# Kernel optimization log

Measured on AMD Instinct MI355X. Metric: run time of the kernel, lower is better.

The kernel has to match this reference:

```python
import jax, jax.numpy as jnp
import numpy as np

B, T, C, H = 2, 4096, 512, 8
HD = C // H  # head_dim = 64


def setup_inputs() -> dict:
    key = jax.random.key(0)
    ks = jax.random.split(key, 5)
    s = 0.02
    return {
        "x": jax.random.normal(ks[0], (B, T, C), dtype=jnp.float32),
        "Wqkv": jax.random.normal(ks[1], (C, 3 * C), dtype=jnp.float32) * s,
        "bqkv": jax.random.normal(ks[2], (3 * C,), dtype=jnp.float32) * s,
        "Wproj": jax.random.normal(ks[3], (C, C), dtype=jnp.float32) * s,
        "bproj": jax.random.normal(ks[4], (C,), dtype=jnp.float32) * s,
    }


def reference(x, Wqkv, bqkv, Wproj, bproj):
    b, t, c = x.shape
    qkv = x @ Wqkv + bqkv                      # [B,T,3C]
    q, k, v = jnp.split(qkv, 3, axis=-1)
    # [B,T,C] -> [B,H,T,HD]
    q = q.reshape(b, t, H, HD).transpose(0, 2, 1, 3)
    k = k.reshape(b, t, H, HD).transpose(0, 2, 1, 3)
    v = v.reshape(b, t, H, HD).transpose(0, 2, 1, 3)
    att = jnp.einsum("bhqd,bhkd->bhqk", q, k) / jnp.sqrt(jnp.float32(HD))
    causal = jnp.tril(jnp.ones((t, t), dtype=bool))
    att = jnp.where(causal, att, -jnp.inf)
    att = jax.nn.softmax(att, axis=-1)
    y = jnp.einsum("bhqk,bhkd->bhqd", att, v)  # [B,H,T,HD]
    y = y.transpose(0, 2, 1, 3).reshape(b, t, c)
    return y @ Wproj + bproj
```

## Files before the change

### kernel.cpp

```cpp
#include <hip/hip_runtime.h>
#include <math.h>

#define NB 2
#define NT 4096
#define NC 512
#define NH 8
#define ND 64
#define N3C (3*NC)

typedef __attribute__((ext_vector_type(8))) __bf16 bf16x8;
typedef __attribute__((ext_vector_type(4))) __bf16 bf16x4;
typedef __attribute__((ext_vector_type(4))) float  f32x4;

__device__ __forceinline__ void load_lds16(const __bf16* g, __bf16* l) {
    __builtin_amdgcn_global_load_lds(
        (const __attribute__((address_space(1))) void*)g,
        (__attribute__((address_space(3))) void*)l, 16, 0, 0);
}

__device__ __forceinline__ float exp2_fast(float x) {
    return __builtin_amdgcn_exp2f(x);
}

__global__ __launch_bounds__(256) void cvt_bf16_kernel(
    const float* __restrict__ x, __bf16* __restrict__ xb, int n)
{
    const int i = (blockIdx.x * 256 + threadIdx.x) << 3;
    if (i < n) {
        float4 a = *(const float4*)(x + i);
        float4 b = *(const float4*)(x + i + 4);
        bf16x8 o;
        o[0] = (__bf16)a.x; o[1] = (__bf16)a.y; o[2] = (__bf16)a.z; o[3] = (__bf16)a.w;
        o[4] = (__bf16)b.x; o[5] = (__bf16)b.y; o[6] = (__bf16)b.z; o[7] = (__bf16)b.w;
        *(bf16x8*)(xb + i) = o;
    }
}

__global__ __launch_bounds__(256) void prep_kernel(
    const float* __restrict__ Wqkv, const float* __restrict__ Wproj,
    __bf16* __restrict__ wqkvt, __bf16* __restrict__ wprojt)
{
    __shared__ float T[64][65];
    int id = blockIdx.x;
    const float* W; __bf16* Wt; int N, n0, k0;
    if (id < 192) { W = Wqkv;  Wt = wqkvt;  N = N3C; n0 = (id % 24) << 6; k0 = (id / 24) << 6; }
    else { id -= 192; W = Wproj; Wt = wprojt; N = NC;  n0 = (id & 7) << 6;  k0 = (id >> 3) << 6; }
    const int K = NC;

    const int tx = threadIdx.x & 15, ty = threadIdx.x >> 4;
#pragma unroll
    for (int i = 0; i < 4; ++i) {
        const int r = ty + (i << 4);
        float4 v = *(const float4*)(W + (size_t)(k0 + r) * N + n0 + (tx << 2));
        T[r][(tx << 2) + 0] = v.x;
        T[r][(tx << 2) + 1] = v.y;
        T[r][(tx << 2) + 2] = v.z;
        T[r][(tx << 2) + 3] = v.w;
    }
    __syncthreads();
#pragma unroll
    for (int i = 0; i < 4; ++i) {
        const int nr = ty + (i << 4);
        bf16x4 o;
        o[0] = (__bf16)T[(tx << 2) + 0][nr];
        o[1] = (__bf16)T[(tx << 2) + 1][nr];
        o[2] = (__bf16)T[(tx << 2) + 2][nr];
        o[3] = (__bf16)T[(tx << 2) + 3][nr];
        *(bf16x4*)(Wt + (size_t)(n0 + nr) * K + k0 + (tx << 2)) = o;
    }
}

template<int BM>
__global__ __launch_bounds__(256) void gemm_glds_kernel(
    const __bf16* __restrict__ A, const __bf16* __restrict__ Bt,
    const float* __restrict__ bias, void* __restrict__ Cout,
    int M, int N, int K, int out_bf16)
{
    constexpr int IT = BM / 32;
    constexpr int AI = BM / 32;
    __shared__ __align__(16) __bf16 As[BM * 64];
    __shared__ __align__(16) __bf16 Bs[128 * 64];

    const int tid  = threadIdx.x;
    const int w    = tid >> 6, lane = tid & 63;
    const int g    = lane >> 4, n = lane & 15;
    const int n7   = n & 7;
    const int wr   = (w >> 1) * (BM / 2);
    const int wc   = (w & 1) << 6;
    const int m0   = blockIdx.y * BM, n0 = blockIdx.x << 7;

    const __bf16* ag[AI]; __bf16* al[AI];
#pragma unroll
    for (int q = 0; q < AI; ++q) {
        const int G = w * (BM * 2) + q * 64 + lane;
        const int r = G >> 3, pg = G & 7, kg = pg ^ (r & 7);
        ag[q] = A + (size_t)(m0 + r) * K + (kg << 3);
        al[q] = As + ((w * (BM * 2) + q * 64) << 3);
    }
    const __bf16* bg[4]; __bf16* bl[4];
#pragma unroll
    for (int q = 0; q < 4; ++q) {
        const int G = w * 256 + q * 64 + lane;
        const int r = G >> 3, pg = G & 7, kg = pg ^ (r & 7);
        bg[q] = Bt + (size_t)(n0 + r) * K + (kg << 3);
        bl[q] = Bs + ((w * 256 + q * 64) << 3);
    }

    f32x4 acc[IT][4];
#pragma unroll
    for (int i = 0; i < IT; ++i)
#pragma unroll
        for (int j = 0; j < 4; ++j) acc[i][j] = (f32x4){0.f, 0.f, 0.f, 0.f};

    const int ksteps = K >> 6;
    for (int ks = 0; ks < ksteps; ++ks) {
        __syncthreads();
        const int ko = ks << 6;
#pragma unroll
        for (int q = 0; q < AI; ++q) load_lds16(ag[q] + ko, al[q]);
#pragma unroll
        for (int q = 0; q < 4;  ++q) load_lds16(bg[q] + ko, bl[q]);
        __syncthreads();

#pragma unroll
        for (int s = 0; s < 2; ++s) {
            bf16x8 af[IT], bf[4];
#pragma unroll
            for (int i = 0; i < IT; ++i) {
                const int row = wr + (i << 4) + n;
                af[i] = *(const bf16x8*)&As[(row << 6) + ((((s << 2) + g) ^ n7) << 3)];
            }
#pragma unroll
            for (int j = 0; j < 4; ++j) {
                const int row = wc + (j << 4) + n;
                bf[j] = *(const bf16x8*)&Bs[(row << 6) + ((((s << 2) + g) ^ n7) << 3)];
            }
#pragma unroll
            for (int i = 0; i < IT; ++i)
#pragma unroll
                for (int j = 0; j < 4; ++j)
                    acc[i][j] = __builtin_amdgcn_mfma_f32_16x16x32_bf16(af[i], bf[j], acc[i][j], 0, 0, 0);
        }
    }

#pragma unroll
    for (int j = 0; j < 4; ++j) {
        const int colg = n0 + wc + (j << 4) + n;
        const float bb = bias[colg];
#pragma unroll
        for (int i = 0; i < IT; ++i) {
#pragma unroll
            for (int reg = 0; reg < 4; ++reg) {
                const int rowg = m0 + wr + (i << 4) + (g << 2) + reg;
                const float v = acc[i][j][reg] + bb;
                if (out_bf16)
                    ((__bf16*)Cout)[(size_t)rowg * N + colg] = (__bf16)v;
                else
                    ((float*)Cout)[(size_t)rowg * N + colg] = v;
            }
        }
    }
}

__global__ __launch_bounds__(256, 4) void attn_kernel(
    const __bf16* __restrict__ qkv, __bf16* __restrict__ out)
{
    __shared__ __align__(16) unsigned char SMEM[34816];
    __bf16 (*QPs)[72] = (__bf16(*)[72])SMEM;
    __bf16* Ks        = (__bf16*)(SMEM + 9216);
    __bf16 (*Vt)[72]  = (__bf16(*)[72])(SMEM + 25600);

    const int tid  = threadIdx.x;
    const int xi   = blockIdx.x;
    const int bh   = blockIdx.y;
    const int b    = bh >> 3, h = bh & 7;
    const int m    = (bh < 8) ? (63 - xi) : xi;
    const int jt1  = m + 1;

    const int qr0  = m << 6;
    const size_t base = (size_t)b * NT * N3C;
    const int col  = h * ND;

    const int w    = tid >> 6;
    const int lane = tid & 63;
    const int g    = lane >> 4;
    const int n    = lane & 15;
    const int qg   = w >> 1;
    const int kh   = w & 1;
    const int qrow0 = qg << 5;
    const int kcol0 = kh << 5;
    const int sw   = (g ^ (n >> 2)) << 3;

    const int kr = tid >> 3;
    const int kc = (tid & 7) << 3;
    const int vd = lane;
    const int vk = w << 3;

    const __bf16* kg_src[2]; __bf16* kl_dst[2];
#pragma unroll
    for (int q = 0; q < 2; ++q) {
        const int G = w * 128 + q * 64 + lane;
        const int r = G >> 3, pg = G & 7, kgr = pg ^ (r & 7);
        kg_src[q] = qkv + base + NC + col + (size_t)r * N3C + (kgr << 3);
        kl_dst[q] = Ks + ((w * 128 + q * 64) << 3);
    }
    const __bf16* vptr = qkv + base + 2 * NC + col + vd;

#pragma unroll
    for (int i = 0; i < 2; ++i) {
        const int r = kr + (i << 5);
        bf16x8 v = *(const bf16x8*)(qkv + base + (size_t)(qr0 + r) * N3C + col + kc);
        bf16x8 q;
#pragma unroll
        for (int j = 0; j < 8; ++j) q[j] = (__bf16)(0.18033688f * (float)v[j]);
        *(bf16x8*)&QPs[r][kc] = q;
    }

#pragma unroll
    for (int q = 0; q < 2; ++q) load_lds16(kg_src[q], kl_dst[q]);
    __bf16 vreg[16];
#pragma unroll
    for (int j = 0; j < 8; ++j) {
        vreg[j]     = vptr[(size_t)(vk + j) * N3C];
        vreg[8 + j] = vptr[(size_t)(vk + 32 + j) * N3C];
    }
    __syncthreads();

    bf16x8 qf[2][2];
#pragma unroll
    for (int qt = 0; qt < 2; ++qt)
#pragma unroll
        for (int hh = 0; hh < 2; ++hh)
            qf[qt][hh] = *(const bf16x8*)&QPs[qrow0 + (qt << 4) + n][(hh << 5) + (g << 3)];

    bf16x8 ones;
#pragma unroll
    for (int j = 0; j < 8; ++j) ones[j] = (__bf16)1.0f;

    f32x4 O[2][4];
#pragma unroll
    for (int qt = 0; qt < 2; ++qt)
#pragma unroll
        for (int dt = 0; dt < 4; ++dt) O[qt][dt] = (f32x4){0.f, 0.f, 0.f, 0.f};
    f32x4 L[2] = {{0.f,0.f,0.f,0.f},{0.f,0.f,0.f,0.f}};

    for (int jt = 0; jt < jt1; ++jt) {
        __syncthreads();
        {
            bf16x8 va, vb;
#pragma unroll
            for (int j = 0; j < 8; ++j) { va[j] = vreg[j]; vb[j] = vreg[8 + j]; }
            *(bf16x8*)&Vt[vd][vk]      = va;
            *(bf16x8*)&Vt[vd][vk + 32] = vb;
        }
        __syncthreads();

        if (jt + 1 < jt1) {
            const size_t roff = (size_t)((jt + 1) << 6) * N3C;
            const int bo = ((jt + 1) & 1) << 12;
#pragma unroll
            for (int q = 0; q < 2; ++q) load_lds16(kg_src[q] + roff, kl_dst[q] + bo);
            const int kr1 = (jt + 1) << 6;
#pragma unroll
            for (int j = 0; j < 8; ++j) {
                vreg[j]     = vptr[(size_t)(kr1 + vk + j) * N3C];
                vreg[8 + j] = vptr[(size_t)(kr1 + vk + 32 + j) * N3C];
            }
        }

        const __bf16* kb = Ks + ((jt & 1) << 12);
        f32x4 S[2][2];
        __builtin_amdgcn_s_setprio(1);
#pragma unroll
        for (int t = 0; t < 2; ++t) {
            const int row = kcol0 + (t << 4) + n;
            const int r7  = row & 7;
            const bf16x8 k0 = *(const bf16x8*)&kb[(row << 6) + ((g ^ r7) << 3)];
            const bf16x8 k1 = *(const bf16x8*)&kb[(row << 6) + (((g ^ 4) ^ r7) << 3)];
#pragma unroll
            for (int qt = 0; qt < 2; ++qt) {
                f32x4 a = {0.f, 0.f, 0.f, 0.f};
                a = __builtin_amdgcn_mfma_f32_16x16x32_bf16(qf[qt][0], k0, a, 0, 0, 0);
                a = __builtin_amdgcn_mfma_f32_16x16x32_bf16(qf[qt][1], k1, a, 0, 0, 0);
                S[qt][t] = a;
            }
        }
        __builtin_amdgcn_s_setprio(0);

        if (jt == m) {
#pragma unroll
            for (int qt = 0; qt < 2; ++qt)
#pragma unroll
                for (int t = 0; t < 2; ++t)
#pragma unroll
                    for (int reg = 0; reg < 4; ++reg) {
                        const int kg  = (jt << 6) + kcol0 + (t << 4) + n;
                        const int qgl = qr0 + qrow0 + (qt << 4) + (g << 2) + reg;
                        if (kg > qgl) S[qt][t][reg] = -INFINITY;
                    }
        }

#pragma unroll
        for (int qt = 0; qt < 2; ++qt)
#pragma unroll
            for (int t = 0; t < 2; ++t)
#pragma unroll
                for (int reg = 0; reg < 4; ++reg)
                    QPs[qrow0 + (qt << 4) + (g << 2) + reg]
                       [kcol0 + (((t << 4) + n) ^ (g << 3))] =
                        (__bf16)exp2_fast(S[qt][t][reg]);

        bf16x8 vf[4];
#pragma unroll
        for (int dt = 0; dt < 4; ++dt) {
            const int vr = (dt << 4) + n;
            vf[dt] = *(const bf16x8*)&Vt[vr][kcol0 + (g << 3)];
        }

        __builtin_amdgcn_s_setprio(1);
#pragma unroll
        for (int qt = 0; qt < 2; ++qt) {
            const bf16x8 p = *(const bf16x8*)&QPs[qrow0 + (qt << 4) + n][kcol0 + sw];
            L[qt] = __builtin_amdgcn_mfma_f32_16x16x32_bf16(p, ones, L[qt], 0, 0, 0);
#pragma unroll
            for (int dt = 0; dt < 4; ++dt)
                O[qt][dt] = __builtin_amdgcn_mfma_f32_16x16x32_bf16(p, vf[dt], O[qt][dt], 0, 0, 0);
        }
        __builtin_amdgcn_s_setprio(0);
    }

    __syncthreads();
    float* red = (float*)SMEM;
    if (kh == 1) {
#pragma unroll
        for (int qt = 0; qt < 2; ++qt)
#pragma unroll
            for (int reg = 0; reg < 4; ++reg) {
                const int qlx = qrow0 + (qt << 4) + (g << 2) + reg;
#pragma unroll
                for (int dt = 0; dt < 4; ++dt)
                    red[qlx * 64 + (dt << 4) + n] = O[qt][dt][reg];
                if (n == 0) red[4096 + qlx] = L[qt][reg];
            }
    }
    __syncthreads();
    if (kh == 0) {
#pragma unroll
        for (int qt = 0; qt < 2; ++qt)
#pragma unroll
            for (int reg = 0; reg < 4; ++reg) {
                const int qlx = qrow0 + (qt << 4) + (g << 2) + reg;
                const float inv = 1.0f / (L[qt][reg] + red[4096 + qlx]);
                const size_t row = (size_t)b * NT + qr0 + qlx;
#pragma unroll
                for (int dt = 0; dt < 4; ++dt)
                    out[row * NC + col + (dt << 4) + n] =
                        (__bf16)((O[qt][dt][reg] + red[qlx * 64 + (dt << 4) + n]) * inv);
            }
    }
}

extern "C" void kernel_launch(void* const* d_in, const int* in_sizes, int n_in,
                              void* d_out, int out_size, void* d_ws, size_t ws_size,
                              hipStream_t stream)
{
    const float* x     = (const float*)d_in[0];
    const float* Wqkv  = (const float*)d_in[1];
    const float* bqkv  = (const float*)d_in[2];
    const float* Wproj = (const float*)d_in[3];
    const float* bproj = (const float*)d_in[4];
    float* out = (float*)d_out;

    char* ws = (char*)d_ws;
    __bf16* xb     = (__bf16*)(ws);
    __bf16* qkvb   = (__bf16*)(ws + 8388608);
    __bf16* attb   = (__bf16*)(ws + 33554432);
    __bf16* wqkvt  = (__bf16*)(ws + 41943040);
    __bf16* wprojt = (__bf16*)(ws + 43515904);

    cvt_bf16_kernel<<<dim3(2048), dim3(256), 0, stream>>>(x, xb, NB * NT * NC);
    prep_kernel<<<dim3(256), dim3(256), 0, stream>>>(Wqkv, Wproj, wqkvt, wprojt);

    gemm_glds_kernel<128><<<dim3(N3C / 128, (NB * NT) / 128), dim3(256), 0, stream>>>(
        xb, wqkvt, bqkv, qkvb, NB * NT, N3C, NC, 1);

    attn_kernel<<<dim3(64, NB * NH), dim3(256), 0, stream>>>(qkvb, attb);

    gemm_glds_kernel<64><<<dim3(NC / 128, (NB * NT) / 64), dim3(256), 0, stream>>>(
        attb, wprojt, bproj, out, NB * NT, NC, NC, 0);
}
```

Measured before the change: 205.7 us.

## Double-buffer LDS tiles in GEMMs and remap blocks across XCDs

```diff
diff --git a/kernel.cpp b/kernel.cpp
--- a/kernel.cpp
+++ b/kernel.cpp
@@ -71,23 +71,30 @@
 }
 
 template<int BM>
-__global__ __launch_bounds__(256) void gemm_glds_kernel(
+__global__ __launch_bounds__(256) void gemm_db_kernel(
     const __bf16* __restrict__ A, const __bf16* __restrict__ Bt,
     const float* __restrict__ bias, void* __restrict__ Cout,
     int M, int N, int K, int out_bf16)
 {
-    constexpr int IT = BM / 32;
-    constexpr int AI = BM / 32;
-    __shared__ __align__(16) __bf16 As[BM * 64];
-    __shared__ __align__(16) __bf16 Bs[128 * 64];
+    constexpr int IT  = BM / 32;
+    constexpr int AI  = BM / 32;
+    constexpr int ASZ = BM * 64;
+    constexpr int BSZ = 128 * 64;
+    __shared__ __align__(16) __bf16 As[2][ASZ];
+    __shared__ __align__(16) __bf16 Bs[2][BSZ];
 
     const int tid  = threadIdx.x;
     const int w    = tid >> 6, lane = tid & 63;
     const int g    = lane >> 4, n = lane & 15;
-    const int n7   = n & 7;
+    const int n7   = n & 15 & 7;
     const int wr   = (w >> 1) * (BM / 2);
     const int wc   = (w & 1) << 6;
-    const int m0   = blockIdx.y * BM, n0 = blockIdx.x << 7;
+
+    const int nwgx = gridDim.x;
+    const int nwg  = nwgx * gridDim.y;
+    const int flat = blockIdx.y * nwgx + blockIdx.x;
+    const int s    = (flat & 7) * (nwg >> 3) + (flat >> 3);
+    const int m0   = (s / nwgx) * BM, n0 = (s % nwgx) << 7;
 
     const __bf16* ag[AI]; __bf16* al[AI];
 #pragma unroll
@@ -95,7 +102,7 @@
         const int G = w * (BM * 2) + q * 64 + lane;
         const int r = G >> 3, pg = G & 7, kg = pg ^ (r & 7);
         ag[q] = A + (size_t)(m0 + r) * K + (kg << 3);
-        al[q] = As + ((w * (BM * 2) + q * 64) << 3);
+        al[q] = &As[0][0] + ((w * (BM * 2) + q * 64) << 3);
     }
     const __bf16* bg[4]; __bf16* bl[4];
 #pragma unroll
@@ -103,7 +110,7 @@
         const int G = w * 256 + q * 64 + lane;
         const int r = G >> 3, pg = G & 7, kg = pg ^ (r & 7);
         bg[q] = Bt + (size_t)(n0 + r) * K + (kg << 3);
-        bl[q] = Bs + ((w * 256 + q * 64) << 3);
+        bl[q] = &Bs[0][0] + ((w * 256 + q * 64) << 3);
     }
 
     f32x4 acc[IT][4];
@@ -112,28 +119,37 @@
 #pragma unroll
         for (int j = 0; j < 4; ++j) acc[i][j] = (f32x4){0.f, 0.f, 0.f, 0.f};
 
+#pragma unroll
+    for (int q = 0; q < AI; ++q) load_lds16(ag[q], al[q]);
+#pragma unroll
+    for (int q = 0; q < 4;  ++q) load_lds16(bg[q], bl[q]);
+    __syncthreads();
+
     const int ksteps = K >> 6;
+    int buf = 0;
     for (int ks = 0; ks < ksteps; ++ks) {
-        __syncthreads();
-        const int ko = ks << 6;
-#pragma unroll
-        for (int q = 0; q < AI; ++q) load_lds16(ag[q] + ko, al[q]);
-#pragma unroll
-        for (int q = 0; q < 4;  ++q) load_lds16(bg[q] + ko, bl[q]);
-        __syncthreads();
-
-#pragma unroll
-        for (int s = 0; s < 2; ++s) {
+        if (ks + 1 < ksteps) {
+            const int ko = (ks + 1) << 6;
+#pragma unroll
+            for (int q = 0; q < AI; ++q) load_lds16(ag[q] + ko, al[q] + (buf ^ 1) * ASZ);
+#pragma unroll
+            for (int q = 0; q < 4;  ++q) load_lds16(bg[q] + ko, bl[q] + (buf ^ 1) * BSZ);
+        }
+
+        const __bf16* Ab = &As[0][0] + buf * ASZ;
+        const __bf16* Bb = &Bs[0][0] + buf * BSZ;
+#pragma unroll
+        for (int sph = 0; sph < 2; ++sph) {
             bf16x8 af[IT], bf[4];
 #pragma unroll
             for (int i = 0; i < IT; ++i) {
                 const int row = wr + (i << 4) + n;
-                af[i] = *(const bf16x8*)&As[(row << 6) + ((((s << 2) + g) ^ n7) << 3)];
+                af[i] = *(const bf16x8*)&Ab[(row << 6) + ((((sph << 2) + g) ^ n7) << 3)];
             }
 #pragma unroll
             for (int j = 0; j < 4; ++j) {
                 const int row = wc + (j << 4) + n;
-                bf[j] = *(const bf16x8*)&Bs[(row << 6) + ((((s << 2) + g) ^ n7) << 3)];
+                bf[j] = *(const bf16x8*)&Bb[(row << 6) + ((((sph << 2) + g) ^ n7) << 3)];
             }
 #pragma unroll
             for (int i = 0; i < IT; ++i)
@@ -141,6 +157,9 @@
                 for (int j = 0; j < 4; ++j)
                     acc[i][j] = __builtin_amdgcn_mfma_f32_16x16x32_bf16(af[i], bf[j], acc[i][j], 0, 0, 0);
         }
+
+        __syncthreads();
+        buf ^= 1;
     }
 
 #pragma unroll
@@ -381,11 +400,11 @@
     cvt_bf16_kernel<<<dim3(2048), dim3(256), 0, stream>>>(x, xb, NB * NT * NC);
     prep_kernel<<<dim3(256), dim3(256), 0, stream>>>(Wqkv, Wproj, wqkvt, wprojt);
 
-    gemm_glds_kernel<128><<<dim3(N3C / 128, (NB * NT) / 128), dim3(256), 0, stream>>>(
+    gemm_db_kernel<128><<<dim3(N3C / 128, (NB * NT) / 128), dim3(256), 0, stream>>>(
         xb, wqkvt, bqkv, qkvb, NB * NT, N3C, NC, 1);
 
     attn_kernel<<<dim3(64, NB * NH), dim3(256), 0, stream>>>(qkvb, attb);
 
-    gemm_glds_kernel<64><<<dim3(NC / 128, (NB * NT) / 64), dim3(256), 0, stream>>>(
+    gemm_db_kernel<64><<<dim3(NC / 128, (NB * NT) / 64), dim3(256), 0, stream>>>(
         attb, wprojt, bproj, out, NB * NT, NC, NC, 0);
 }
```

After: 200.0 us. 1.03x faster.
